# Optimization experiments

Hardware: AMD Instinct MI355X
Metric: run time of the kernel (lower is better)

Reference implementation:

```python
import jax, jax.numpy as jnp
import numpy as np

B, S, D_IN, D_OUT, H = 2, 2048, 1024, 1024, 16
HD = D_OUT // H


def setup_inputs() -> dict:
    key = jax.random.key(0)
    ks = jax.random.split(key, 6)
    s = 0.02
    return {
        "X": jax.random.normal(ks[0], (B, S, D_IN), dtype=jnp.float32),
        "Wq": jax.random.normal(ks[1], (D_OUT, D_IN), dtype=jnp.float32) * s,
        "Wk": jax.random.normal(ks[2], (D_OUT, D_IN), dtype=jnp.float32) * s,
        "Wv": jax.random.normal(ks[3], (D_OUT, D_IN), dtype=jnp.float32) * s,
        "Wo": jax.random.normal(ks[4], (D_OUT, D_OUT), dtype=jnp.float32) * s,
        "bo": jax.random.normal(ks[5], (D_OUT,), dtype=jnp.float32) * s,
    }


def reference(X, Wq, Wk, Wv, Wo, bo):
    b, n, _ = X.shape
    # torch Linear: y = x @ W^T
    Q = (X @ Wq.T).reshape(b, n, H, HD).transpose(0, 2, 1, 3)  # [b,h,s,hd]
    K = (X @ Wk.T).reshape(b, n, H, HD).transpose(0, 2, 1, 3)
    V = (X @ Wv.T).reshape(b, n, H, HD).transpose(0, 2, 1, 3)
    S_ = jnp.einsum('bhqd,bhkd->bhqk', Q, K)  # [b,h,s,s]
    causal = jnp.triu(jnp.ones((n, n), dtype=bool), k=1)
    S_ = jnp.where(causal, -jnp.inf, S_)
    W = jax.nn.softmax(S_ / jnp.sqrt(jnp.float32(HD)), axis=-1)
    Z = jnp.einsum('bhqk,bhkd->bhqd', W, V)
    Z = Z.transpose(0, 2, 1, 3).reshape(b, n, D_OUT)
    return Z @ Wo.T + bo
```

## Files before the change

kernel.cpp:

```cpp
#include <hip/hip_runtime.h>
#include <stdint.h>

typedef __bf16 bf16x8 __attribute__((ext_vector_type(8)));
typedef float  f32x4  __attribute__((ext_vector_type(4)));
typedef unsigned int u32x4 __attribute__((ext_vector_type(4)));

#define S_   2048
#define DM   1024
#define QSCALE 0.18033688011112042f

__device__ __forceinline__ unsigned short f2b(float f) {
    uint32_t u = __builtin_bit_cast(uint32_t, f);
    u += 0x7fffu + ((u >> 16) & 1u);
    return (unsigned short)(u >> 16);
}

__device__ __forceinline__ uint32_t pack2bf(float a, float b) {
    uint32_t ua = __builtin_bit_cast(uint32_t, a) + 0x8000u;
    uint32_t ub = __builtin_bit_cast(uint32_t, b) + 0x8000u;
    return __builtin_amdgcn_perm(ub, ua, 0x07060302);
}

__device__ __forceinline__ void glds16(const void* g, void* l) {
    __builtin_amdgcn_global_load_lds(
        (const __attribute__((address_space(1))) void*)g,
        (__attribute__((address_space(3))) void*)l, 16, 0, 0);
}

__global__ void cvt_all(const float* __restrict__ X,
                        const float* __restrict__ Wq, const float* __restrict__ Wk,
                        const float* __restrict__ Wv,
                        unsigned short* __restrict__ Xb, unsigned short* __restrict__ Wb)
{
    size_t i = ((size_t)blockIdx.x * 256 + threadIdx.x) * 4;
    const float* src;
    unsigned short* dst;
    size_t off;
    if (i < (size_t)4194304) { src = X; dst = Xb; off = i; }
    else {
        size_t j = i - 4194304;
        int sel = (int)(j >> 20);
        off = j & 1048575;
        src = (sel == 0) ? Wq : (sel == 1) ? Wk : Wv;
        dst = Wb + (size_t)sel * 1048576;
    }
    float4 v = *(const float4*)&src[off];
    uint2 o;
    o.x = pack2bf(v.x, v.y);
    o.y = pack2bf(v.z, v.w);
    *(uint2*)&dst[off] = o;
}

__global__ __launch_bounds__(256, 2)
void qkv_gemm(const unsigned short* __restrict__ Xb,
              const unsigned short* __restrict__ Wqb,
              const unsigned short* __restrict__ Wkb,
              const unsigned short* __restrict__ Wvb,
              unsigned short* __restrict__ Qo, unsigned short* __restrict__ Ko,
              unsigned short* __restrict__ Vto)
{
    __shared__ unsigned short Ash[128 * 32];
    __shared__ unsigned short Bsh[128 * 32];

    const int t = threadIdx.x;
    const int lane = t & 63, w = t >> 6;
    const int lcol = lane & 15, quad = lane >> 4;
    const int z = blockIdx.z;
    const int rowBase = ((z == 2) ? blockIdx.y : blockIdx.x) * 128;
    const int colBase = ((z == 2) ? blockIdx.x : blockIdx.y) * 128;
    const unsigned short* aPtr = (z == 2) ? Wvb : Xb;
    const unsigned short* bPtr = (z == 0) ? Wqb : (z == 1) ? Wkb : Xb;
    const int wr = (w >> 1) * 64, wc = (w & 1) * 64;

    f32x4 acc[4][4];
    #pragma unroll
    for (int i = 0; i < 4; ++i)
        #pragma unroll
        for (int j = 0; j < 4; ++j) acc[i][j] = (f32x4){0.f,0.f,0.f,0.f};

    for (int k0 = 0; k0 < DM; k0 += 32) {
        __syncthreads();
        #pragma unroll
        for (int p = 0; p < 2; ++p) {
            int ci = p * 256 + t;
            glds16(&aPtr[(size_t)(rowBase + (ci >> 2)) * DM + k0 + (ci & 3) * 8], &Ash[ci * 8]);
        }
        #pragma unroll
        for (int p = 0; p < 2; ++p) {
            int ci = p * 256 + t;
            glds16(&bPtr[(size_t)(colBase + (ci >> 2)) * DM + k0 + (ci & 3) * 8], &Bsh[ci * 8]);
        }
        __syncthreads();
        bf16x8 af[4], bfr[4];
        #pragma unroll
        for (int i = 0; i < 4; ++i) af[i]  = *(const bf16x8*)&Ash[(wr + i*16 + lcol)*32 + quad*8];
        #pragma unroll
        for (int i = 0; i < 4; ++i) bfr[i] = *(const bf16x8*)&Bsh[(wc + i*16 + lcol)*32 + quad*8];
        #pragma unroll
        for (int i = 0; i < 4; ++i)
            #pragma unroll
            for (int j = 0; j < 4; ++j)
                acc[i][j] = __builtin_amdgcn_mfma_f32_16x16x32_bf16(af[i], bfr[j], acc[i][j], 0, 0, 0);
    }

    unsigned short* Cm = (z == 0) ? Qo : (z == 1) ? Ko : Vto;
    const int ld = (z == 2) ? (S_ * 2) : DM;
    const float sc = (z == 0) ? QSCALE : 1.0f;
    #pragma unroll
    for (int i = 0; i < 4; ++i)
        #pragma unroll
        for (int j = 0; j < 4; ++j)
            #pragma unroll
            for (int r = 0; r < 4; ++r) {
                int row = rowBase + wr + i*16 + quad*4 + r;
                int col = colBase + wc + j*16 + lcol;
                Cm[(size_t)row * ld + col] = f2b(acc[i][j][r] * sc);
            }
}

__global__ __launch_bounds__(512, 4)
void attn_kernel(const unsigned short* __restrict__ Q,
                 const unsigned short* __restrict__ K,
                 const unsigned short* __restrict__ Vt,
                 unsigned short* __restrict__ Z)
{
    __shared__ __align__(16) unsigned short SH[18432];

    const int t = threadIdx.x;
    const int lane = t & 63, w = t >> 6;
    const int lcol = lane & 15, quad = lane >> 4;
    const int kh = w & 1, wq = w >> 1;

    const int bh = blockIdx.x;
    const int b = bh >> 4, h = bh & 15;
    const int y = blockIdx.y;
    const int tile = (y < 8) ? (15 - y) : (y - 8);
    const int q0 = tile * 128;
    const int nchunk = 2 * tile + 2;

    const unsigned short* Qg = Q + (size_t)(b * S_ + q0) * DM + h * 64;
    const unsigned short* Kg = K + (size_t)(b * S_) * DM + h * 64;
    const unsigned short* Vg = Vt + (size_t)(h * 64) * (S_ * 2) + b * S_;

    bf16x8 qf[2][2];
    #pragma unroll
    for (int qi = 0; qi < 2; ++qi)
        #pragma unroll
        for (int kd = 0; kd < 2; ++kd)
            qf[qi][kd] = *(const bf16x8*)&Qg[(size_t)(wq*32 + qi*16 + lcol) * DM + kd*32 + quad*8];

    bool mk[4];
    #pragma unroll
    for (int r = 0; r < 4; ++r) mk[r] = (quad*4 + r) > lcol;

    float lp[2] = {0.f, 0.f};
    f32x4 o[2][4];
    #pragma unroll
    for (int qi = 0; qi < 2; ++qi)
        #pragma unroll
        for (int nd = 0; nd < 4; ++nd) o[qi][nd] = (f32x4){0.f,0.f,0.f,0.f};

    const int sr = t >> 3, sch = t & 7;

    {
        uint4 k0 = *(const uint4*)&Kg[(size_t)sr * DM + sch * 8];
        uint4 v0 = *(const uint4*)&Vg[(size_t)sr * (S_ * 2) + sch * 8];
        *(uint4*)&SH[sr * 72 + sch * 8] = k0;
        *(uint4*)&SH[9216 + sr * 72 + sch * 8] = v0;
    }
    __syncthreads();

    const int Qb0 = tile * 8 + wq * 2;
    const int gq = ((quad & 1) << 1) | (quad >> 1);
    const bool qodd = (quad & 1) != 0;

    for (int c = 0; c < nchunk; ++c) {
        const int cur = c & 1;
        const bool pf = (c + 1 < nchunk);
        uint4 kn, vn;
        if (pf) {
            const int kc1 = (c + 1) * 64;
            kn = *(const uint4*)&Kg[(size_t)(kc1 + sr) * DM + sch * 8];
            vn = *(const uint4*)&Vg[(size_t)sr * (S_ * 2) + kc1 + sch * 8];
        }
        const unsigned short* Kc = &SH[cur * 4608];
        const unsigned short* Vc = &SH[9216 + cur * 4608];

        const int Kb0 = c * 4 + kh * 2;
        if (Kb0 <= Qb0 + 1) {
            uint32_t pw[2][2][2];
            #pragma unroll
            for (int nk = 0; nk < 2; ++nk) {
                const int Kb = Kb0 + nk;
                if (Kb <= Qb0 + 1) {
                    bf16x8 ak0 = *(const bf16x8*)&Kc[(kh*32 + nk*16 + lcol)*72 + quad*8];
                    bf16x8 ak1 = *(const bf16x8*)&Kc[(kh*32 + nk*16 + lcol)*72 + 32 + quad*8];
                    #pragma unroll
                    for (int qi = 0; qi < 2; ++qi) {
                        if (Kb <= Qb0 + qi) {
                            f32x4 s = (f32x4){0.f,0.f,0.f,0.f};
                            s = __builtin_amdgcn_mfma_f32_16x16x32_bf16(ak0, qf[qi][0], s, 0, 0, 0);
                            s = __builtin_amdgcn_mfma_f32_16x16x32_bf16(ak1, qf[qi][1], s, 0, 0, 0);
                            float p0 = __builtin_amdgcn_exp2f(s[0]);
                            float p1 = __builtin_amdgcn_exp2f(s[1]);
                            float p2 = __builtin_amdgcn_exp2f(s[2]);
                            float p3 = __builtin_amdgcn_exp2f(s[3]);
                            if (Kb == Qb0 + qi) {
                                p0 = mk[0] ? 0.f : p0;
                                p1 = mk[1] ? 0.f : p1;
                                p2 = mk[2] ? 0.f : p2;
                                p3 = mk[3] ? 0.f : p3;
                            }
                            lp[qi] += (p0 + p1) + (p2 + p3);
                            pw[qi][nk][0] = pack2bf(p0, p1);
                            pw[qi][nk][1] = pack2bf(p2, p3);
                        } else {
                            pw[qi][nk][0] = 0u;
                            pw[qi][nk][1] = 0u;
                        }
                    }
                } else {
                    #pragma unroll
                    for (int qi = 0; qi < 2; ++qi) {
                        pw[qi][nk][0] = 0u;
                        pw[qi][nk][1] = 0u;
                    }
                }
            }

            bf16x8 ap[2];
            #pragma unroll
            for (int qi = 0; qi < 2; ++qi) {
                uint32_t a0 = pw[qi][0][0], a1 = pw[qi][0][1];
                uint32_t b0 = pw[qi][1][0], b1 = pw[qi][1][1];
                uint32_t xa0 = (uint32_t)__shfl_xor((int)a0, 16);
                uint32_t xa1 = (uint32_t)__shfl_xor((int)a1, 16);
                uint32_t xb0 = (uint32_t)__shfl_xor((int)b0, 16);
                uint32_t xb1 = (uint32_t)__shfl_xor((int)b1, 16);
                u32x4 apw;
                apw[0] = qodd ? xb0 : a0;
                apw[1] = qodd ? xb1 : a1;
                apw[2] = qodd ? b0 : xa0;
                apw[3] = qodd ? b1 : xa1;
                ap[qi] = __builtin_bit_cast(bf16x8, apw);
            }

            #pragma unroll
            for (int nd = 0; nd < 4; ++nd) {
                bf16x8 bv = *(const bf16x8*)&Vc[(nd*16 + lcol)*72 + kh*32 + gq*8];
                #pragma unroll
                for (int qi = 0; qi < 2; ++qi)
                    o[qi][nd] = __builtin_amdgcn_mfma_f32_16x16x32_bf16(ap[qi], bv, o[qi][nd], 0, 0, 0);
            }
        }

        if (pf) {
            *(uint4*)&SH[(cur ^ 1) * 4608 + sr * 72 + sch * 8] = kn;
            *(uint4*)&SH[9216 + (cur ^ 1) * 4608 + sr * 72 + sch * 8] = vn;
        }
        __syncthreads();
    }

    #pragma unroll
    for (int qi = 0; qi < 2; ++qi) {
        lp[qi] += __shfl_xor(lp[qi], 16);
        lp[qi] += __shfl_xor(lp[qi], 32);
    }
    float* red = (float*)SH;
    float* my = red + (wq * 64 + lane) * 36;
    if (kh == 1) {
        #pragma unroll
        for (int qi = 0; qi < 2; ++qi)
            #pragma unroll
            for (int nd = 0; nd < 4; ++nd)
                *(f32x4*)&my[qi*16 + nd*4] = o[qi][nd];
        my[32] = lp[0];
        my[33] = lp[1];
    }
    __syncthreads();
    if (kh == 0) {
        #pragma unroll
        for (int qi = 0; qi < 2; ++qi)
            #pragma unroll
            for (int nd = 0; nd < 4; ++nd)
                o[qi][nd] += *(const f32x4*)&my[qi*16 + nd*4];
        float linv[2];
        linv[0] = 1.0f / (lp[0] + my[32]);
        linv[1] = 1.0f / (lp[1] + my[33]);
        #pragma unroll
        for (int qi = 0; qi < 2; ++qi)
            #pragma unroll
            for (int r = 0; r < 4; ++r) {
                float lr = __shfl(linv[qi], quad*4 + r);
                unsigned short* Zr = Z + (size_t)(b*S_ + q0 + wq*32 + qi*16 + quad*4 + r) * DM + h*64;
                #pragma unroll
                for (int nd = 0; nd < 4; ++nd)
                    Zr[nd*16 + lcol] = f2b(o[qi][nd][r] * lr);
            }
    }
}

__global__ __launch_bounds__(256, 2)
void out_gemm(const unsigned short* __restrict__ A,
              const float* __restrict__ Wo, const float* __restrict__ bo,
              float* __restrict__ Out)
{
    __shared__ unsigned short Ash[128 * 32];
    __shared__ unsigned short Bsh[128 * 32];

    const int t = threadIdx.x;
    const int lane = t & 63, w = t >> 6;
    const int lcol = lane & 15, quad = lane >> 4;
    const int rowBase = blockIdx.x * 128;
    const int colBase = blockIdx.y * 128;
    const int wr = (w >> 1) * 64, wc = (w & 1) * 64;

    f32x4 acc[4][4];
    #pragma unroll
    for (int i = 0; i < 4; ++i)
        #pragma unroll
        for (int j = 0; j < 4; ++j) acc[i][j] = (f32x4){0.f,0.f,0.f,0.f};

    for (int k0 = 0; k0 < DM; k0 += 32) {
        __syncthreads();
        #pragma unroll
        for (int p = 0; p < 2; ++p) {
            int ci = p * 256 + t;
            glds16(&A[(size_t)(rowBase + (ci >> 2)) * DM + k0 + (ci & 3) * 8], &Ash[ci * 8]);
        }
        #pragma unroll
        for (int p = 0; p < 2; ++p) {
            int c = p * 256 + t;
            int row = c >> 2, col = (c & 3) * 8;
            const float* ws_ = &Wo[(size_t)(colBase + row) * DM + k0 + col];
            float4 fa = *(const float4*)&ws_[0];
            float4 fb = *(const float4*)&ws_[4];
            uint4 wv;
            wv.x = pack2bf(fa.x, fa.y);
            wv.y = pack2bf(fa.z, fa.w);
            wv.z = pack2bf(fb.x, fb.y);
            wv.w = pack2bf(fb.z, fb.w);
            *(uint4*)&Bsh[row * 32 + col] = wv;
        }
        __syncthreads();
        bf16x8 af[4], bfr[4];
        #pragma unroll
        for (int i = 0; i < 4; ++i) af[i]  = *(const bf16x8*)&Ash[(wr + i*16 + lcol)*32 + quad*8];
        #pragma unroll
        for (int j = 0; j < 4; ++j) bfr[j] = *(const bf16x8*)&Bsh[(wc + j*16 + lcol)*32 + quad*8];
        #pragma unroll
        for (int i = 0; i < 4; ++i)
            #pragma unroll
            for (int j = 0; j < 4; ++j)
                acc[i][j] = __builtin_amdgcn_mfma_f32_16x16x32_bf16(af[i], bfr[j], acc[i][j], 0, 0, 0);
    }

    float bb[4];
    #pragma unroll
    for (int j = 0; j < 4; ++j) bb[j] = bo[colBase + wc + j*16 + lcol];

    #pragma unroll
    for (int i = 0; i < 4; ++i)
        #pragma unroll
        for (int j = 0; j < 4; ++j)
            #pragma unroll
            for (int r = 0; r < 4; ++r) {
                int row = rowBase + wr + i*16 + quad*4 + r;
                int col = colBase + wc + j*16 + lcol;
                Out[(size_t)row * DM + col] = acc[i][j][r] + bb[j];
            }
}

extern "C" void kernel_launch(void* const* d_in, const int* in_sizes, int n_in,
                              void* d_out, int out_size, void* d_ws, size_t ws_size,
                              hipStream_t stream) {
    const float* X  = (const float*)d_in[0];
    const float* Wq = (const float*)d_in[1];
    const float* Wk = (const float*)d_in[2];
    const float* Wv = (const float*)d_in[3];
    const float* Wo = (const float*)d_in[4];
    const float* bo = (const float*)d_in[5];
    float* out = (float*)d_out;

    unsigned short* Xb  = (unsigned short*)d_ws;
    unsigned short* Qw  = Xb + (size_t)4096 * 1024;
    unsigned short* Kw  = Qw + (size_t)4096 * 1024;
    unsigned short* Vtw = Kw + (size_t)4096 * 1024;
    unsigned short* Zb  = Xb;
    unsigned short* Wb  = (unsigned short*)d_out;

    cvt_all<<<dim3(7168), 256, 0, stream>>>(X, Wq, Wk, Wv, Xb, Wb);
    qkv_gemm<<<dim3(32, 8, 3), 256, 0, stream>>>(Xb, Wb, Wb + (size_t)1048576,
                                                 Wb + (size_t)2097152, Qw, Kw, Vtw);
    attn_kernel<<<dim3(32, 16), 512, 0, stream>>>(Qw, Kw, Vtw, Zb);
    out_gemm<<<dim3(32, 8), 256, 0, stream>>>(Zb, Wo, bo, out);
}
```

Measured before the change: 186.9 us.

## Double-buffer out_gemm shared tiles and use 512 threads per block

Rewrites the output-projection GEMM to double-buffer its A and Wo tiles in shared memory. The next K-slice is loaded and prefetched while MFMAs run on the current one, which removes one barrier per iteration. The block grows to 8 waves, each computing a 32x64 sub-tile instead of 64x64, so each thread issues one load per operand instead of two. This hides global-load latency and raises wave count, at the cost of doubled shared memory and less register-level reuse per wave.

New measurement: 183.0 us. 2.0% less time.

```diff
diff --git a/kernel.cpp b/kernel.cpp
--- a/kernel.cpp
+++ b/kernel.cpp
@@ -300,59 +300,75 @@
     }
 }
 
-__global__ __launch_bounds__(256, 2)
+__global__ __launch_bounds__(512, 2)
 void out_gemm(const unsigned short* __restrict__ A,
               const float* __restrict__ Wo, const float* __restrict__ bo,
               float* __restrict__ Out)
 {
-    __shared__ unsigned short Ash[128 * 32];
-    __shared__ unsigned short Bsh[128 * 32];
+    __shared__ unsigned short Ash[2][128 * 32];
+    __shared__ unsigned short Bsh[2][128 * 32];
 
     const int t = threadIdx.x;
     const int lane = t & 63, w = t >> 6;
     const int lcol = lane & 15, quad = lane >> 4;
     const int rowBase = blockIdx.x * 128;
     const int colBase = blockIdx.y * 128;
-    const int wr = (w >> 1) * 64, wc = (w & 1) * 64;
-
-    f32x4 acc[4][4];
-    #pragma unroll
-    for (int i = 0; i < 4; ++i)
+    const int wr = (w >> 1) * 32, wc = (w & 1) * 64;
+
+    const int srow = t >> 2, scol = (t & 3) * 8;
+
+    f32x4 acc[2][4];
+    #pragma unroll
+    for (int i = 0; i < 2; ++i)
         #pragma unroll
         for (int j = 0; j < 4; ++j) acc[i][j] = (f32x4){0.f,0.f,0.f,0.f};
 
-    for (int k0 = 0; k0 < DM; k0 += 32) {
-        __syncthreads();
-        #pragma unroll
-        for (int p = 0; p < 2; ++p) {
-            int ci = p * 256 + t;
-            glds16(&A[(size_t)(rowBase + (ci >> 2)) * DM + k0 + (ci & 3) * 8], &Ash[ci * 8]);
-        }
-        #pragma unroll
-        for (int p = 0; p < 2; ++p) {
-            int c = p * 256 + t;
-            int row = c >> 2, col = (c & 3) * 8;
-            const float* ws_ = &Wo[(size_t)(colBase + row) * DM + k0 + col];
-            float4 fa = *(const float4*)&ws_[0];
-            float4 fb = *(const float4*)&ws_[4];
+    {
+        glds16(&A[(size_t)(rowBase + srow) * DM + scol], &Ash[0][t * 8]);
+        const float* ws_ = &Wo[(size_t)(colBase + srow) * DM + scol];
+        float4 fa = *(const float4*)&ws_[0];
+        float4 fb = *(const float4*)&ws_[4];
+        uint4 wv;
+        wv.x = pack2bf(fa.x, fa.y);
+        wv.y = pack2bf(fa.z, fa.w);
+        wv.z = pack2bf(fb.x, fb.y);
+        wv.w = pack2bf(fb.z, fb.w);
+        *(uint4*)&Bsh[0][t * 8] = wv;
+    }
+    __syncthreads();
+
+    for (int ks = 0; ks < 32; ++ks) {
+        const int cur = ks & 1;
+        const bool pf = (ks + 1 < 32);
+        float4 fa, fb;
+        if (pf) {
+            const int k1 = (ks + 1) * 32;
+            glds16(&A[(size_t)(rowBase + srow) * DM + k1 + scol], &Ash[cur ^ 1][t * 8]);
+            const float* ws_ = &Wo[(size_t)(colBase + srow) * DM + k1 + scol];
+            fa = *(const float4*)&ws_[0];
+            fb = *(const float4*)&ws_[4];
+        }
+
+        bf16x8 af[2], bfr[4];
+        #pragma unroll
+        for (int i = 0; i < 2; ++i) af[i]  = *(const bf16x8*)&Ash[cur][(wr + i*16 + lcol)*32 + quad*8];
+        #pragma unroll
+        for (int j = 0; j < 4; ++j) bfr[j] = *(const bf16x8*)&Bsh[cur][(wc + j*16 + lcol)*32 + quad*8];
+        #pragma unroll
+        for (int i = 0; i < 2; ++i)
+            #pragma unroll
+            for (int j = 0; j < 4; ++j)
+                acc[i][j] = __builtin_amdgcn_mfma_f32_16x16x32_bf16(af[i], bfr[j], acc[i][j], 0, 0, 0);
+
+        if (pf) {
             uint4 wv;
             wv.x = pack2bf(fa.x, fa.y);
             wv.y = pack2bf(fa.z, fa.w);
             wv.z = pack2bf(fb.x, fb.y);
             wv.w = pack2bf(fb.z, fb.w);
-            *(uint4*)&Bsh[row * 32 + col] = wv;
+            *(uint4*)&Bsh[cur ^ 1][t * 8] = wv;
         }
         __syncthreads();
-        bf16x8 af[4], bfr[4];
-        #pragma unroll
-        for (int i = 0; i < 4; ++i) af[i]  = *(const bf16x8*)&Ash[(wr + i*16 + lcol)*32 + quad*8];
-        #pragma unroll
-        for (int j = 0; j < 4; ++j) bfr[j] = *(const bf16x8*)&Bsh[(wc + j*16 + lcol)*32 + quad*8];
-        #pragma unroll
-        for (int i = 0; i < 4; ++i)
-            #pragma unroll
-            for (int j = 0; j < 4; ++j)
-                acc[i][j] = __builtin_amdgcn_mfma_f32_16x16x32_bf16(af[i], bfr[j], acc[i][j], 0, 0, 0);
     }
 
     float bb[4];
@@ -360,7 +376,7 @@
     for (int j = 0; j < 4; ++j) bb[j] = bo[colBase + wc + j*16 + lcol];
 
     #pragma unroll
-    for (int i = 0; i < 4; ++i)
+    for (int i = 0; i < 2; ++i)
         #pragma unroll
         for (int j = 0; j < 4; ++j)
             #pragma unroll
@@ -393,5 +409,5 @@
     qkv_gemm<<<dim3(32, 8, 3), 256, 0, stream>>>(Xb, Wb, Wb + (size_t)1048576,
                                                  Wb + (size_t)2097152, Qw, Kw, Vtw);
     attn_kernel<<<dim3(32, 16), 512, 0, stream>>>(Qw, Kw, Vtw, Zb);
-    out_gemm<<<dim3(32, 8), 256, 0, stream>>>(Zb, Wo, bo, out);
-}
+    out_gemm<<<dim3(32, 8), 512, 0, stream>>>(Zb, Wo, bo, out);
+}
```
